# Kernel tuning notes

Hardware: AMD Instinct MI355X
Metric: run time of the kernel (lower is better)

## Reference

```python
import jax, jax.numpy as jnp
import numpy as np

B, N, DIM = 4, 2048, 3
H = 128          # hidden
K = 32           # num_neighbours
L = 4            # num_layers
OUT = 6          # out_per_particle


def _dense_init(key, fan_in, fan_out):
    kw, kb = jax.random.split(key)
    w = jax.random.normal(kw, (fan_in, fan_out), jnp.float32) / np.sqrt(fan_in)
    b = jnp.zeros((fan_out,), jnp.float32)
    return w, b


def setup_inputs() -> dict:
    key = jax.random.key(0)
    ks = jax.random.split(key, 8)
    x = jax.random.normal(ks[0], (B, N, DIM), jnp.float32)
    embed_w, embed_b = _dense_init(ks[1], DIM, H)
    # per-layer stacked params
    miw, mib, mow, mob, uiw, uib, uow, uob = [], [], [], [], [], [], [], []
    for l in range(L):
        k0, k1, k2, k3 = jax.random.split(jax.random.fold_in(ks[2], l), 4)
        w, b = _dense_init(k0, 2 * H + 1, H); miw.append(w); mib.append(b)
        w, b = _dense_init(k1, H, H);         mow.append(w); mob.append(b)
        w, b = _dense_init(k2, 2 * H, H);     uiw.append(w); uib.append(b)
        w, b = _dense_init(k3, H, H);         uow.append(w); uob.append(b)
    out_w, out_b = _dense_init(ks[3], H, OUT)
    return {
        'x': x,
        'embed_w': embed_w, 'embed_b': embed_b,
        'msg_in_w': jnp.stack(miw), 'msg_in_b': jnp.stack(mib),
        'msg_out_w': jnp.stack(mow), 'msg_out_b': jnp.stack(mob),
        'upd_in_w': jnp.stack(uiw), 'upd_in_b': jnp.stack(uib),
        'upd_out_w': jnp.stack(uow), 'upd_out_b': jnp.stack(uob),
        'out_w': out_w, 'out_b': out_b,
    }


def reference(x, embed_w, embed_b,
              msg_in_w, msg_in_b, msg_out_w, msg_out_b,
              upd_in_w, upd_in_b, upd_out_w, upd_out_b,
              out_w, out_b):
    act = jax.nn.silu
    n = x.shape[-2]
    # per-particle embed: (B,N,H)
    h = x @ embed_w + embed_b
    # pairwise squared distances (B,N,N), plain Euclidean (geometry=None)
    diff = x[..., :, None, :] - x[..., None, :, :]
    d_sq = jnp.sum(diff * diff, axis=-1)
    eye = jnp.eye(n, dtype=bool)
    d_sq = jnp.where(eye, jnp.inf, d_sq)
    neg_topk, idx_topk = jax.lax.top_k(-d_sq, K)      # (B,N,K)
    d_nearest = jnp.sqrt(jnp.maximum(-neg_topk, 0.0))  # (B,N,K)

    gather = jax.vmap(lambda hb, ib: hb[ib])  # (N,H),(N,K)->(N,K,H) over batch
    n_layers = msg_in_w.shape[0]
    for l in range(n_layers):
        nb = gather(h, idx_topk)                               # (B,N,K,H)
        node_i = jnp.broadcast_to(h[..., :, None, :], nb.shape)
        msg_inp = jnp.concatenate([node_i, nb, d_nearest[..., None]], axis=-1)
        msg = act(msg_inp @ msg_in_w[l] + msg_in_b[l]) @ msg_out_w[l] + msg_out_b[l]
        agg = jnp.sum(msg, axis=-2)                            # (B,N,H)
        upd_inp = jnp.concatenate([h, agg], axis=-1)
        upd = act(upd_inp @ upd_in_w[l] + upd_in_b[l]) @ upd_out_w[l] + upd_out_b[l]
        h = h + upd
    return h @ out_w + out_b
```

## Files before the change

kernel.cpp:

```cpp
#include <hip/hip_runtime.h>
#include <math.h>

#define B_ 4
#define N_ 2048
#define H_ 128
#define K_ 32
#define L_ 4
#define OUT_ 6
#define BN_ (B_*N_)
#define NPB_L 16
#define LBLK 512

typedef __attribute__((ext_vector_type(8))) short short8;
typedef __attribute__((ext_vector_type(4))) float f32x4;

#define LDW (H_ + 8)
#define LAYER_W 98304
#define OFF_W1A 0
#define OFF_W1C 16384
#define OFF_W2  32768
#define OFF_U1  49152
#define OFF_U2  81920
#define SCAP 256
#define KNN_ROWS 4
#define KNN_BLKS (BN_/KNN_ROWS)
#define PREP_BLKS (L_*LAYER_W/256)

#define LOG2E 1.44269504088896340736f
#define LN2   0.69314718055994530942f

__device__ __forceinline__ float silu_f(float x) {
    float e = __builtin_amdgcn_exp2f(-x * LOG2E);
    return x * __builtin_amdgcn_rcpf(1.0f + e);
}
__device__ __forceinline__ short f2b(float f) {
    unsigned u = __float_as_uint(f);
    return (short)((u + 0x7FFFu + ((u >> 16) & 1u)) >> 16);
}
__device__ __forceinline__ unsigned pack2(short lo, short hi) {
    return (unsigned)(unsigned short)lo | ((unsigned)(unsigned short)hi << 16);
}
__device__ __forceinline__ int mbcnt64(unsigned long long m) {
    return __builtin_amdgcn_mbcnt_hi((unsigned)(m >> 32),
           __builtin_amdgcn_mbcnt_lo((unsigned)m, 0));
}

__global__ __launch_bounds__(256) void k_front(
    const float* __restrict__ x, int* __restrict__ nidx, float* __restrict__ ndist,
    const float* __restrict__ miw, const float* __restrict__ mow,
    const float* __restrict__ uiw, const float* __restrict__ uow,
    short* __restrict__ wt,
    const float* __restrict__ ew, const float* __restrict__ eb,
    const float* __restrict__ mib, float* __restrict__ Epack)
{
    __shared__ float xsx[N_], xsy[N_], xsz[N_];
    __shared__ unsigned skey[KNN_ROWS][SCAP];
    __shared__ int      sid [KNN_ROWS][SCAP];

    if (blockIdx.x >= KNN_BLKS + PREP_BLKS) {
        int t = threadIdx.x;
        int which = t >> 7, n = t & 127;
        const float* W = miw + (size_t)(which ? 128 : 0) * H_;
        float E0 = 0.f, E1 = 0.f, E2 = 0.f, Eb = 0.f;
        for (int k = 0; k < 128; ++k) {
            float w = W[(size_t)k*H_ + n];
            E0 = fmaf(ew[k],       w, E0);
            E1 = fmaf(ew[128 + k], w, E1);
            E2 = fmaf(ew[256 + k], w, E2);
            Eb = fmaf(eb[k],       w, Eb);
        }
        float* dst = Epack + which * 512;
        dst[0*128 + n] = E0 * LOG2E;
        dst[1*128 + n] = E1 * LOG2E;
        dst[2*128 + n] = E2 * LOG2E;
        dst[3*128 + n] = (Eb + (which ? 0.f : mib[n])) * LOG2E;
        return;
    }
    if (blockIdx.x >= KNN_BLKS) {
        int gid = (blockIdx.x - KNN_BLKS) * 256 + threadIdx.x;
        int l = gid / LAYER_W, o = gid - l * LAYER_W;
        float v;
        if (o < OFF_W1C) {
            int n = o >> 7, k = o & 127;
            v = miw[(size_t)l*257*H_ + k*H_ + n] * LOG2E;
        } else if (o < OFF_W2) {
            int oo = o - OFF_W1C, n = oo >> 7, k = oo & 127;
            v = miw[(size_t)l*257*H_ + (128 + k)*H_ + n] * LOG2E;
        } else if (o < OFF_U1) {
            int oo = o - OFF_W2, n = oo >> 7, k = oo & 127;
            v = mow[(size_t)l*H_*H_ + k*H_ + n];
        } else if (o < OFF_U2) {
            int oo = o - OFF_U1, n = oo >> 8, k = oo & 255;
            v = uiw[(size_t)l*2*H_*H_ + k*H_ + n];
        } else {
            int oo = o - OFF_U2, n = oo >> 7, k = oo & 127;
            v = uow[(size_t)l*H_*H_ + k*H_ + n];
        }
        wt[gid] = f2b(v);
        return;
    }

    int b  = blockIdx.x / (N_/KNN_ROWS);
    int i0 = (blockIdx.x % (N_/KNN_ROWS)) * KNN_ROWS;
    const float* xb = x + (size_t)b*N_*3;
    for (int t = threadIdx.x; t < N_*3; t += 256) {
        float v = xb[t];
        int q = t / 3, r = t - q*3;
        float* dst = (r == 0) ? xsx : (r == 1) ? xsy : xsz;
        dst[q] = v;
    }
    __syncthreads();

    int wave = threadIdx.x >> 6, lane = threadIdx.x & 63;
    int i = i0 + wave;
    float xix = xsx[i], xiy = xsy[i], xiz = xsz[i];

    unsigned u[N_/64];
    unsigned lmin = 0xFFFFFFFFu;
#pragma unroll
    for (int t = 0; t < N_/64; ++t) {
        int j = lane + 64*t;
        float d0 = xix-xsx[j], d1 = xiy-xsy[j], d2 = xiz-xsz[j];
        float d = d0*d0 + d1*d1 + d2*d2;
        unsigned k = (j == i) ? 0x7F800000u : __float_as_uint(d);
        u[t] = k;
        lmin = min(lmin, k);
    }
    unsigned mn = lmin, mx = lmin;
    for (int off = 32; off; off >>= 1) {
        unsigned o1 = (unsigned)__shfl_xor((int)mn, off); mn = min(mn, o1);
        unsigned o2 = (unsigned)__shfl_xor((int)mx, off); mx = max(mx, o2);
    }
    unsigned Tup = mn;
    if (mn != mx) {
        int hb = 31 - __clz((int)(mn ^ mx));
        Tup = mn & ~((2u << hb) - 1u);
        for (int bit = hb; bit >= 0; --bit) {
            unsigned cand = Tup | (1u << bit);
            if (__popcll(__ballot(lmin < cand)) < K_) Tup = cand;
        }
    }
    unsigned* sk = skey[wave];
    int*      si = sid [wave];
    int base = 0;
#pragma unroll
    for (int t = 0; t < N_/64; ++t) {
        bool pr = (u[t] <= Tup);
        unsigned long long m = __ballot(pr);
        if (pr) {
            int pos = base + mbcnt64(m);
            if (pos < SCAP) { sk[pos] = u[t]; si[pos] = lane + 64*t; }
        }
        base += __popcll(m);
    }
    int c = min(base, SCAP);
    unsigned sv[4]; int iv[4];
#pragma unroll
    for (int q = 0; q < 4; ++q) {
        int slot = lane + 64*q;
        bool ok = slot < c;
        sv[q] = ok ? sk[slot] : 0xFFFFFFFFu;
        iv[q] = ok ? si[slot] : 0;
    }
    unsigned T = mn;
    if (mn != Tup) {
        int hb = 31 - __clz((int)(mn ^ Tup));
        T = mn & ~((2u << hb) - 1u);
        for (int bit = hb; bit >= 0; --bit) {
            unsigned cand = T | (1u << bit);
            int cnt = __popcll(__ballot(sv[0] < cand)) + __popcll(__ballot(sv[1] < cand))
                    + __popcll(__ballot(sv[2] < cand)) + __popcll(__ballot(sv[3] < cand));
            if (cnt < K_) T = cand;
        }
    }
    int cnt_lt = __popcll(__ballot(sv[0] < T)) + __popcll(__ballot(sv[1] < T))
               + __popcll(__ballot(sv[2] < T)) + __popcll(__ballot(sv[3] < T));
    int need = K_ - cnt_lt;
    size_t rbase = ((size_t)(b*N_ + i)) * K_;
    int ltc = 0, eqc = 0;
#pragma unroll
    for (int q = 0; q < 4; ++q) {
        bool lt = sv[q] < T, eq = sv[q] == T;
        unsigned long long mlt = __ballot(lt), meq = __ballot(eq);
        int pp = ltc + mbcnt64(mlt), ee = eqc + mbcnt64(meq);
        ltc += __popcll(mlt); eqc += __popcll(meq);
        int pos = lt ? pp : ((eq && ee < need) ? (cnt_lt + ee) : -1);
        if (pos >= 0) {
            nidx [rbase + pos] = iv[q];
            ndist[rbase + pos] = sqrtf(__uint_as_float(sv[q]));
        }
    }
}

__global__ __launch_bounds__(512) void k_prep0(
    float* __restrict__ h, short* __restrict__ a, short* __restrict__ c0,
    const float* __restrict__ x, const float* __restrict__ ew,
    const float* __restrict__ eb, const float* __restrict__ Epack)
{
    int t = blockIdx.x * 512 + threadIdx.x;
    int node = t >> 7, ch = t & 127;
    const float* xp = x + (size_t)node*3;
    float x0 = xp[0], x1 = xp[1], x2 = xp[2];
    float hv = eb[ch];
    hv = fmaf(x0, ew[ch],       hv);
    hv = fmaf(x1, ew[H_+ch],    hv);
    hv = fmaf(x2, ew[2*H_+ch],  hv);
    float av = Epack[384+ch];
    av = fmaf(x0, Epack[ch],     av);
    av = fmaf(x1, Epack[128+ch], av);
    av = fmaf(x2, Epack[256+ch], av);
    float cv = Epack[896+ch];
    cv = fmaf(x0, Epack[512+ch], cv);
    cv = fmaf(x1, Epack[640+ch], cv);
    cv = fmaf(x2, Epack[768+ch], cv);
    size_t gi = (size_t)node*H_ + ch;
    h[gi]  = hv;
    a[gi]  = f2b(av);
    c0[gi] = f2b(cv);
}

__global__ __launch_bounds__(LBLK, 4) void k_layer(
    float* __restrict__ h, short* __restrict__ a,
    const int* __restrict__ nidx, const float* __restrict__ ndist,
    const float* __restrict__ wd,
    const short* __restrict__ wl,
    const float* __restrict__ b2, const float* __restrict__ u1b,
    const float* __restrict__ u2b,
    const short* __restrict__ c_rd, short* __restrict__ c_wr,
    const short* __restrict__ wn, const float* __restrict__ b1n, int do_ac,
    const float* __restrict__ ow, const float* __restrict__ ob,
    float* __restrict__ out)
{
    __shared__ __align__(16) short s_l[NPB_L][LDW];
    __shared__ __align__(16) short h_l[NPB_L][LDW];
    __shared__ __align__(16) short agg_l[NPB_L][LDW];
    __shared__ __align__(16) float h32s[NPB_L][H_];
    __shared__ int   idx_s[NPB_L][K_];
    __shared__ float dst_s[NPB_L][K_];
    int blk = blockIdx.x;
    int batch = (blk & 7) >> 1;
    int sub   = ((blk >> 3) << 1) | (blk & 1);
    int node0 = batch * N_ + sub * NPB_L;
    int tid = threadIdx.x;
    int wave = tid >> 6, lane = tid & 63, l15 = lane & 15, quad = lane >> 4;
    int ncol = wave*16 + l15;

    {
        float4 v = reinterpret_cast<const float4*>(h + (size_t)node0*H_)[tid];
        int row = tid >> 5, col = (tid & 31) * 4;
        h_l[row][col+0] = f2b(v.x); h_l[row][col+1] = f2b(v.y);
        h_l[row][col+2] = f2b(v.z); h_l[row][col+3] = f2b(v.w);
        *(float4*)&h32s[row][col] = v;
    }
    idx_s[tid>>5][tid&31] = nidx[(size_t)node0*K_ + tid];
    dst_s[tid>>5][tid&31] = ndist[(size_t)node0*K_ + tid];
    __syncthreads();

    {
        float wd0 = wd[2*lane] * LOG2E, wd1 = wd[2*lane+1] * LOG2E;
        int wavu = __builtin_amdgcn_readfirstlane(wave);
        const unsigned* c2 = (const unsigned*)c_rd + (size_t)batch*N_*(H_/2);
        const unsigned* a2 = (const unsigned*)a;
        for (int nn = 0; nn < 2; ++nn) {
            int m = wavu*2 + nn;
            unsigned av = a2[(size_t)(node0+m)*(H_/2) + lane];
            float a0 = __uint_as_float(av << 16);
            float a1 = __uint_as_float(av & 0xFFFF0000u);
            float s0 = 0.f, s1 = 0.f;
            for (int kc = 0; kc < K_; kc += 8) {
                unsigned cv[8];
#pragma unroll
                for (int k = 0; k < 8; ++k) {
                    int j = __builtin_amdgcn_readfirstlane(idx_s[m][kc + k]);
                    cv[k] = c2[(size_t)j*(H_/2) + lane];
                }
#pragma unroll
                for (int k = 0; k < 8; ++k) {
                    float dd = dst_s[m][kc + k];
                    float y0 = a0 + fmaf(dd, wd0, __uint_as_float(cv[k] << 16));
                    float y1 = a1 + fmaf(dd, wd1, __uint_as_float(cv[k] & 0xFFFF0000u));
                    float t0 = __builtin_amdgcn_rcpf(1.0f + __builtin_amdgcn_exp2f(-y0));
                    float t1 = __builtin_amdgcn_rcpf(1.0f + __builtin_amdgcn_exp2f(-y1));
                    s0 = fmaf(y0, t0, s0);
                    s1 = fmaf(y1, t1, s1);
                }
            }
            *(unsigned*)&s_l[m][2*lane] = pack2(f2b(s0 * LN2), f2b(s1 * LN2));
        }
    }
    __syncthreads();

    f32x4 acc;
    acc = (f32x4){0,0,0,0};
#pragma unroll
    for (int kk = 0; kk < 4; ++kk) {
        int k0 = kk*32 + quad*8;
        short8 bf = *(const short8*)(wl + OFF_W2 + (size_t)ncol*H_ + k0);
        short8 af = *(const short8*)&s_l[l15][k0];
        acc = __builtin_amdgcn_mfma_f32_16x16x32_bf16(af, bf, acc, 0, 0, 0);
    }
    {
        float b2v = b2[ncol] * (float)K_;
#pragma unroll
        for (int r = 0; r < 4; ++r)
            agg_l[quad*4 + r][ncol] = f2b(acc[r] + b2v);
    }
    __syncthreads();

    acc = (f32x4){0,0,0,0};
#pragma unroll
    for (int kk = 0; kk < 8; ++kk) {
        const short (*src)[LDW] = (kk < 4) ? h_l : agg_l;
        int kloc = ((kk < 4) ? kk*32 : (kk-4)*32) + quad*8;
        short8 bf = *(const short8*)(wl + OFF_U1 + (size_t)ncol*2*H_ + kk*32 + quad*8);
        short8 af = *(const short8*)&src[l15][kloc];
        acc = __builtin_amdgcn_mfma_f32_16x16x32_bf16(af, bf, acc, 0, 0, 0);
    }
    {
        float u1bv = u1b[ncol];
#pragma unroll
        for (int r = 0; r < 4; ++r)
            s_l[quad*4 + r][ncol] = f2b(silu_f(acc[r] + u1bv));
    }
    __syncthreads();

    acc = (f32x4){0,0,0,0};
#pragma unroll
    for (int kk = 0; kk < 4; ++kk) {
        int k0 = kk*32 + quad*8;
        short8 bf = *(const short8*)(wl + OFF_U2 + (size_t)ncol*H_ + k0);
        short8 af = *(const short8*)&s_l[l15][k0];
        acc = __builtin_amdgcn_mfma_f32_16x16x32_bf16(af, bf, acc, 0, 0, 0);
    }
    {
        float u2bv = u2b[ncol];
#pragma unroll
        for (int r = 0; r < 4; ++r) {
            int m = quad*4 + r;
            float nh = h32s[m][ncol] + acc[r] + u2bv;
            h[(size_t)(node0+m)*H_ + ncol] = nh;
            if (do_ac) h_l[m][ncol] = f2b(nh);
            else       h32s[m][ncol] = nh;
        }
    }
    if (do_ac) {
        __syncthreads();
        int n = ncol;
        f32x4 accA = (f32x4){0,0,0,0}, accC = (f32x4){0,0,0,0};
#pragma unroll
        for (int kk = 0; kk < 4; ++kk) {
            int k0 = kk*32 + quad*8;
            short8 af = *(const short8*)&h_l[l15][k0];
            short8 bA = *(const short8*)(wn + OFF_W1A + (size_t)ncol*H_ + k0);
            short8 bC = *(const short8*)(wn + OFF_W1C + (size_t)ncol*H_ + k0);
            accA = __builtin_amdgcn_mfma_f32_16x16x32_bf16(af, bA, accA, 0, 0, 0);
            accC = __builtin_amdgcn_mfma_f32_16x16x32_bf16(af, bC, accC, 0, 0, 0);
        }
        float b1v = b1n[n] * LOG2E;
#pragma unroll
        for (int r = 0; r < 4; ++r) {
            int m = quad*4 + r;
            size_t gi = (size_t)(node0+m)*H_ + n;
            a[gi]    = f2b(accA[r] + b1v);
            c_wr[gi] = f2b(accC[r]);
        }
    } else {
        __syncthreads();
        int node = tid >> 5, s = tid & 31;
        float p0=0.f,p1=0.f,p2=0.f,p3=0.f,p4=0.f,p5=0.f;
#pragma unroll
        for (int q = 0; q < 4; ++q) {
            int r = s + q*32;
            float hv = h32s[node][r];
            const float* owr = ow + r*OUT_;
            p0 = fmaf(hv, owr[0], p0); p1 = fmaf(hv, owr[1], p1);
            p2 = fmaf(hv, owr[2], p2); p3 = fmaf(hv, owr[3], p3);
            p4 = fmaf(hv, owr[4], p4); p5 = fmaf(hv, owr[5], p5);
        }
#pragma unroll
        for (int off = 16; off; off >>= 1) {
            p0 += __shfl_xor(p0, off); p1 += __shfl_xor(p1, off);
            p2 += __shfl_xor(p2, off); p3 += __shfl_xor(p3, off);
            p4 += __shfl_xor(p4, off); p5 += __shfl_xor(p5, off);
        }
        if (s == 0) {
            float* op = out + (size_t)(node0+node)*OUT_;
            op[0] = p0 + ob[0]; op[1] = p1 + ob[1]; op[2] = p2 + ob[2];
            op[3] = p3 + ob[3]; op[4] = p4 + ob[4]; op[5] = p5 + ob[5];
        }
    }
}

extern "C" void kernel_launch(void* const* d_in, const int* in_sizes, int n_in,
                              void* d_out, int out_size, void* d_ws, size_t ws_size,
                              hipStream_t stream)
{
    const float* x   = (const float*)d_in[0];
    const float* ew  = (const float*)d_in[1];
    const float* eb  = (const float*)d_in[2];
    const float* miw = (const float*)d_in[3];
    const float* mib = (const float*)d_in[4];
    const float* mow = (const float*)d_in[5];
    const float* mob = (const float*)d_in[6];
    const float* uiw = (const float*)d_in[7];
    const float* uib = (const float*)d_in[8];
    const float* uow = (const float*)d_in[9];
    const float* uob = (const float*)d_in[10];
    const float* ow  = (const float*)d_in[11];
    const float* ob  = (const float*)d_in[12];
    float* out = (float*)d_out;

    char* w = (char*)d_ws;
    float* h  = (float*)w;                         w += (size_t)BN_*H_*4;
    float* nd = (float*)w;                         w += (size_t)BN_*K_*4;
    int*   ni = (int*)w;                           w += (size_t)BN_*K_*4;
    short* a  = (short*)w;                         w += (size_t)BN_*H_*2;
    short* c0 = (short*)w;                         w += (size_t)BN_*H_*2;
    short* c1 = (short*)w;                         w += (size_t)BN_*H_*2;
    short* wt = (short*)w;                         w += (size_t)L_*LAYER_W*2;
    float* Epack = (float*)w;

    k_front<<<KNN_BLKS + PREP_BLKS + 1, 256, 0, stream>>>(x, ni, nd,
        miw, mow, uiw, uow, wt, ew, eb, mib, Epack);
    k_prep0<<<BN_*H_/512, 512, 0, stream>>>(h, a, c0, x, ew, eb, Epack);
    for (int l = 0; l < L_; ++l) {
        const short* c_rd = (l & 1) ? c1 : c0;
        short*       c_wr = (l & 1) ? c0 : c1;
        int do_ac = (l + 1 < L_);
        const short* wn = wt + (size_t)(do_ac ? (l+1) : l) * LAYER_W;
        const float* b1n = mib + (size_t)(do_ac ? (l+1) : l) * H_;
        k_layer<<<BN_/NPB_L, LBLK, 0, stream>>>(h, a, ni, nd,
            miw + (size_t)l*257*H_ + 256*H_,
            wt + (size_t)l*LAYER_W,
            mob + (size_t)l*H_, uib + (size_t)l*H_, uob + (size_t)l*H_,
            c_rd, c_wr, wn, b1n, do_ac,
            ow, ob, out);
    }
}
```

Baseline: 202.7 us.

## Prefetch all neighbour gathers into registers before the sync and barrier

Each wave now loads its 64 neighbour indices directly from global memory into a register and broadcasts them with readlane, which removes the idx_s shared array. All 64 neighbour rows for the wave's two nodes are gathered into registers up front, before the h staging and the barrier, instead of in chunks of 8 inside the loop. The aim is to put far more loads in flight and overlap gather latency with the other setup work. The cost is 64 extra VGPRs per thread, which under launch_bounds(512,4) risks spills or lower occupancy.

```diff
diff --git a/kernel.cpp b/kernel.cpp
--- a/kernel.cpp
+++ b/kernel.cpp
@@ -235,7 +235,6 @@
     __shared__ __align__(16) short h_l[NPB_L][LDW];
     __shared__ __align__(16) short agg_l[NPB_L][LDW];
     __shared__ __align__(16) float h32s[NPB_L][H_];
-    __shared__ int   idx_s[NPB_L][K_];
     __shared__ float dst_s[NPB_L][K_];
     int blk = blockIdx.x;
     int batch = (blk & 7) >> 1;
@@ -244,7 +243,29 @@
     int tid = threadIdx.x;
     int wave = tid >> 6, lane = tid & 63, l15 = lane & 15, quad = lane >> 4;
     int ncol = wave*16 + l15;
-
+    int wavu = __builtin_amdgcn_readfirstlane(wave);
+    int m0 = wavu*2, m1 = m0 + 1;
+
+    int myidx = nidx[(size_t)node0*K_ + tid];
+    float mydst = ndist[(size_t)node0*K_ + tid];
+    const unsigned* c2 = (const unsigned*)c_rd + (size_t)batch*N_*(H_/2);
+    const unsigned* a2 = (const unsigned*)a;
+    unsigned av0 = a2[(size_t)(node0+m0)*(H_/2) + lane];
+    unsigned av1 = a2[(size_t)(node0+m1)*(H_/2) + lane];
+
+    unsigned cv0[K_], cv1[K_];
+#pragma unroll
+    for (int k = 0; k < K_; ++k) {
+        int j = __builtin_amdgcn_readlane(myidx, k);
+        cv0[k] = c2[(size_t)j*(H_/2) + lane];
+    }
+#pragma unroll
+    for (int k = 0; k < K_; ++k) {
+        int j = __builtin_amdgcn_readlane(myidx, 32 + k);
+        cv1[k] = c2[(size_t)j*(H_/2) + lane];
+    }
+
+    dst_s[tid>>5][tid&31] = mydst;
     {
         float4 v = reinterpret_cast<const float4*>(h + (size_t)node0*H_)[tid];
         int row = tid >> 5, col = (tid & 31) * 4;
@@ -252,41 +273,30 @@
         h_l[row][col+2] = f2b(v.z); h_l[row][col+3] = f2b(v.w);
         *(float4*)&h32s[row][col] = v;
     }
-    idx_s[tid>>5][tid&31] = nidx[(size_t)node0*K_ + tid];
-    dst_s[tid>>5][tid&31] = ndist[(size_t)node0*K_ + tid];
     __syncthreads();
 
     {
         float wd0 = wd[2*lane] * LOG2E, wd1 = wd[2*lane+1] * LOG2E;
-        int wavu = __builtin_amdgcn_readfirstlane(wave);
-        const unsigned* c2 = (const unsigned*)c_rd + (size_t)batch*N_*(H_/2);
-        const unsigned* a2 = (const unsigned*)a;
-        for (int nn = 0; nn < 2; ++nn) {
-            int m = wavu*2 + nn;
-            unsigned av = a2[(size_t)(node0+m)*(H_/2) + lane];
-            float a0 = __uint_as_float(av << 16);
-            float a1 = __uint_as_float(av & 0xFFFF0000u);
-            float s0 = 0.f, s1 = 0.f;
-            for (int kc = 0; kc < K_; kc += 8) {
-                unsigned cv[8];
-#pragma unroll
-                for (int k = 0; k < 8; ++k) {
-                    int j = __builtin_amdgcn_readfirstlane(idx_s[m][kc + k]);
-                    cv[k] = c2[(size_t)j*(H_/2) + lane];
-                }
-#pragma unroll
-                for (int k = 0; k < 8; ++k) {
-                    float dd = dst_s[m][kc + k];
-                    float y0 = a0 + fmaf(dd, wd0, __uint_as_float(cv[k] << 16));
-                    float y1 = a1 + fmaf(dd, wd1, __uint_as_float(cv[k] & 0xFFFF0000u));
-                    float t0 = __builtin_amdgcn_rcpf(1.0f + __builtin_amdgcn_exp2f(-y0));
-                    float t1 = __builtin_amdgcn_rcpf(1.0f + __builtin_amdgcn_exp2f(-y1));
-                    s0 = fmaf(y0, t0, s0);
-                    s1 = fmaf(y1, t1, s1);
-                }
-            }
-            *(unsigned*)&s_l[m][2*lane] = pack2(f2b(s0 * LN2), f2b(s1 * LN2));
-        }
+        float a00 = __uint_as_float(av0 << 16);
+        float a01 = __uint_as_float(av0 & 0xFFFF0000u);
+        float a10 = __uint_as_float(av1 << 16);
+        float a11 = __uint_as_float(av1 & 0xFFFF0000u);
+        float s00 = 0.f, s01 = 0.f, s10 = 0.f, s11 = 0.f;
+#pragma unroll
+        for (int k = 0; k < K_; ++k) {
+            float d0 = dst_s[m0][k];
+            float d1 = dst_s[m1][k];
+            float y00 = a00 + fmaf(d0, wd0, __uint_as_float(cv0[k] << 16));
+            float y01 = a01 + fmaf(d0, wd1, __uint_as_float(cv0[k] & 0xFFFF0000u));
+            float y10 = a10 + fmaf(d1, wd0, __uint_as_float(cv1[k] << 16));
+            float y11 = a11 + fmaf(d1, wd1, __uint_as_float(cv1[k] & 0xFFFF0000u));
+            s00 = fmaf(y00, __builtin_amdgcn_rcpf(1.0f + __builtin_amdgcn_exp2f(-y00)), s00);
+            s01 = fmaf(y01, __builtin_amdgcn_rcpf(1.0f + __builtin_amdgcn_exp2f(-y01)), s01);
+            s10 = fmaf(y10, __builtin_amdgcn_rcpf(1.0f + __builtin_amdgcn_exp2f(-y10)), s10);
+            s11 = fmaf(y11, __builtin_amdgcn_rcpf(1.0f + __builtin_amdgcn_exp2f(-y11)), s11);
+        }
+        *(unsigned*)&s_l[m0][2*lane] = pack2(f2b(s00 * LN2), f2b(s01 * LN2));
+        *(unsigned*)&s_l[m1][2*lane] = pack2(f2b(s10 * LN2), f2b(s11 * LN2));
     }
     __syncthreads();
 
```

Result: no change. 206.6 us (+1.9%).
